# Kernel optimization log

Measured on AMD Instinct MI355X. Metric: run time of the kernel, lower is better.

The kernel has to match this reference:

```python
import jax, jax.numpy as jnp
import numpy as np

D_MODEL = 16
D_STATE = 8
D_CONV = 2
EXPAND = 1
HEADDIM = 2
CHUNK = 64
D_INNER = EXPAND * D_MODEL          # 16
NHEADS = D_INNER // HEADDIM         # 8
CONV_DIM = D_INNER + 2 * D_STATE    # 32
D_IN_PROJ = 2 * D_INNER + 2 * D_STATE + NHEADS  # 56
OBS_DIM = 32
N_ACTIONS = 16
T_LEN = 4096
BATCH = 32


def setup_inputs() -> dict:
    key = jax.random.key(0)
    ks = jax.random.split(key, 16)
    return {
        "obs": jax.random.normal(ks[0], (T_LEN, BATCH, OBS_DIM), jnp.float32),
        "W_in": jax.random.normal(ks[1], (D_MODEL, OBS_DIM), jnp.float32) * 0.1,
        "b_in": jax.random.normal(ks[2], (D_MODEL,), jnp.float32) * 0.1,
        "in_proj": jax.random.normal(ks[3], (D_IN_PROJ, D_MODEL), jnp.float32) * 0.1,
        "conv_w": jax.random.normal(ks[4], (CONV_DIM, D_CONV), jnp.float32) * 0.2,
        "conv_b": jax.random.normal(ks[5], (CONV_DIM,), jnp.float32) * 0.1,
        "dt_bias": jax.random.normal(ks[6], (NHEADS,), jnp.float32) * 0.1,
        "A_log": jax.random.normal(ks[7], (NHEADS,), jnp.float32) * 0.5,
        "D_skip": jax.random.normal(ks[8], (NHEADS,), jnp.float32) * 0.1,
        "norm_w": jnp.ones((D_INNER,), jnp.float32),
        "out_proj": jax.random.normal(ks[9], (D_MODEL, D_INNER), jnp.float32) * 0.1,
        "W_out": jax.random.normal(ks[10], (N_ACTIONS, D_MODEL), jnp.float32) * 0.1,
        "b_out": jax.random.normal(ks[11], (N_ACTIONS,), jnp.float32) * 0.1,
    }


def _segsum(x):
    # x: (..., T) -> (..., T, T) with out[..., i, j] = sum_{k=j+1..i} x_k (i>=j), else -inf
    T = x.shape[-1]
    xx = jnp.broadcast_to(x[..., None], x.shape + (T,))
    xx = jnp.where(jnp.tril(jnp.ones((T, T), bool), -1), xx, 0.0)
    s = jnp.cumsum(xx, axis=-2)
    return jnp.where(jnp.tril(jnp.ones((T, T), bool), 0), s, -jnp.inf)


def _ssd(x, A, B, C):
    # x: (b, l, h, p); A: (b, l, h); B, C: (b, l, n). Chunked SSD scan.
    b, l, h, p = x.shape
    c = l // CHUNK
    x = x.reshape(b, c, CHUNK, h, p)
    A = A.reshape(b, c, CHUNK, h).transpose(0, 3, 1, 2)       # b h c l
    B = B.reshape(b, c, CHUNK, -1)                            # b c l n
    C = C.reshape(b, c, CHUNK, -1)                            # b c l n
    A_cs = jnp.cumsum(A, axis=-1)                             # b h c l
    L = jnp.exp(_segsum(A))                                   # b h c l l
    Y_diag = jnp.einsum('bcln,bcsn,bhcls,bcshp->bclhp', C, B, L, x)
    decay_states = jnp.exp(A_cs[..., -1:] - A_cs)             # b h c l
    states = jnp.einsum('bcln,bhcl,bclhp->bchpn', B, decay_states, x)
    states = jnp.concatenate([jnp.zeros_like(states[:, :1]), states], axis=1)  # b (c+1) h p n
    decay_chunk = jnp.exp(_segsum(jnp.pad(A_cs[..., -1], ((0, 0), (0, 0), (1, 0)))))  # b h c+1 c+1
    new_states = jnp.einsum('bhzc,bchpn->bzhpn', decay_chunk, states)
    states = new_states[:, :-1]                               # b c h p n
    Y_off = jnp.einsum('bcln,bchpn,bhcl->bclhp', C, states, jnp.exp(A_cs))
    return (Y_diag + Y_off).reshape(b, l, h, p)


def reference(obs, W_in, b_in, in_proj, conv_w, conv_b, dt_bias, A_log, D_skip,
              norm_w, out_proj, W_out, b_out):
    t, Bsz, _ = obs.shape
    # input Linear + ReLU -> (t, B, d_model); rearrange to (B, t, d_model)
    x = jax.nn.relu(obs @ W_in.T + b_in)
    u = x.transpose(1, 0, 2)                                  # (B, t, d_model)
    zxbcdt = u @ in_proj.T                                    # (B, t, 56)
    z = zxbcdt[..., :D_INNER]
    xBC = zxbcdt[..., D_INNER:D_INNER + CONV_DIM]
    dt = jax.nn.softplus(zxbcdt[..., D_INNER + CONV_DIM:] + dt_bias)  # (B, t, h)
    # causal depthwise conv1d (kernel size D_CONV) + SiLU
    xp = jnp.pad(xBC, ((0, 0), (D_CONV - 1, 0), (0, 0)))
    conv = conv_b
    for k in range(D_CONV):
        conv = conv + xp[:, k:k + t] * conv_w[:, k]
    xBC = jax.nn.silu(conv)
    xs = xBC[..., :D_INNER]
    Bm = xBC[..., D_INNER:D_INNER + D_STATE]
    Cm = xBC[..., D_INNER + D_STATE:]
    A = -jnp.exp(A_log)                                       # (h,)
    xh = xs.reshape(Bsz, t, NHEADS, HEADDIM)
    y = _ssd(xh * dt[..., None], A * dt, Bm, Cm)
    y = y + xh * D_skip[None, None, :, None]
    y = y.reshape(Bsz, t, D_INNER)
    # gated RMSNorm
    y = y * jax.nn.silu(z)
    y = y * jax.lax.rsqrt(jnp.mean(y * y, axis=-1, keepdims=True) + 1e-5) * norm_w
    yo = y @ out_proj.T                                       # (B, t, d_model)
    hid = yo.transpose(1, 0, 2).reshape(t * Bsz, D_MODEL)     # (t*B, n_units)
    logits = jax.nn.relu(hid) @ W_out.T + b_out
    return logits.reshape(t, Bsz, -1)
```

## Files before the change

### kernel.cpp

```cpp
#include <hip/hip_runtime.h>

#define T_LEN  4096
#define BATCHN 32
#define NROWS  (T_LEN*BATCHN)
#define CHUNKL 64
#define NCHUNK (T_LEN/CHUNKL)

#define SIN_STRIDE 52
#define SY_STRIDE  28

typedef float4 f4;

__device__ __forceinline__ float fsilu(float x){ return x / (1.f + __expf(-x)); }
__device__ __forceinline__ float fsoftplus(float x){ return (x > 20.f) ? x : log1pf(__expf(x)); }

__device__ __forceinline__ float group8_sum(float v){
  v += __shfl_xor(v, 1);
  v += __shfl_xor(v, 2);
  v += __shfl_xor(v, 4);
  return v;
}

__global__ __launch_bounds__(256) void k1_proj(
    const float* __restrict__ obs, const float* __restrict__ W_in,
    const float* __restrict__ b_in, const float* __restrict__ in_proj,
    const float* __restrict__ dt_bias,
    float* __restrict__ z_g, float* __restrict__ xbc_g, float* __restrict__ dt_g)
{
  int r = blockIdx.x*256 + threadIdx.x;
  float o[32];
  const f4* op = (const f4*)(obs + (size_t)r*32);
  #pragma unroll
  for (int j=0;j<8;j++){ f4 v = op[j]; o[4*j]=v.x; o[4*j+1]=v.y; o[4*j+2]=v.z; o[4*j+3]=v.w; }
  float x[16];
  #pragma unroll
  for (int i=0;i<16;i++){
    float a = b_in[i];
    #pragma unroll
    for (int k=0;k<32;k++) a += o[k]*W_in[i*32+k];
    x[i] = a > 0.f ? a : 0.f;
  }
  float acc[56];
  #pragma unroll
  for (int j=0;j<56;j++){
    float a = 0.f;
    #pragma unroll
    for (int k=0;k<16;k++) a += x[k]*in_proj[j*16+k];
    acc[j] = a;
  }
  f4* zo = (f4*)(z_g + (size_t)r*16);
  #pragma unroll
  for (int j=0;j<4;j++) zo[j] = make_float4(acc[4*j],acc[4*j+1],acc[4*j+2],acc[4*j+3]);
  f4* xo = (f4*)(xbc_g + (size_t)r*32);
  #pragma unroll
  for (int j=0;j<8;j++) xo[j] = make_float4(acc[16+4*j],acc[17+4*j],acc[18+4*j],acc[19+4*j]);
  float dtv[8];
  #pragma unroll
  for (int k=0;k<8;k++) dtv[k] = fsoftplus(acc[48+k] + dt_bias[k]);
  f4* dto = (f4*)(dt_g + (size_t)r*8);
  dto[0] = make_float4(dtv[0],dtv[1],dtv[2],dtv[3]);
  dto[1] = make_float4(dtv[4],dtv[5],dtv[6],dtv[7]);
}

__global__ __launch_bounds__(64) void k2_scan(
    const float* __restrict__ xbc_g, const float* __restrict__ dt_g,
    const float* __restrict__ conv_w, const float* __restrict__ conv_b,
    const float* __restrict__ A_log, const float* __restrict__ D_skip,
    float* __restrict__ yl_g, float* __restrict__ ea_g, float* __restrict__ cm_g,
    float* __restrict__ sloc_g, float* __restrict__ p_g)
{
  __shared__ float s_in[CHUNKL*SIN_STRIDE];
  __shared__ float s_y[CHUNKL*SY_STRIDE];
  int bid = blockIdx.x;
  int b = bid & 31, c = bid >> 5;
  int l = threadIdx.x;
  int t = c*CHUNKL + l;
  size_t r = (size_t)t*BATCHN + b;

  float xb[32], pv[32], dtv[8];
  {
    const f4* xp = (const f4*)(xbc_g + r*32);
    #pragma unroll
    for (int j=0;j<8;j++){ f4 v=xp[j]; xb[4*j]=v.x; xb[4*j+1]=v.y; xb[4*j+2]=v.z; xb[4*j+3]=v.w; }
    if (t == 0) {
      #pragma unroll
      for (int j=0;j<32;j++) pv[j]=0.f;
    } else {
      const f4* pp = (const f4*)(xbc_g + (r-BATCHN)*32);
      #pragma unroll
      for (int j=0;j<8;j++){ f4 v=pp[j]; pv[4*j]=v.x; pv[4*j+1]=v.y; pv[4*j+2]=v.z; pv[4*j+3]=v.w; }
    }
    const f4* dp = (const f4*)(dt_g + r*8);
    f4 d0=dp[0], d1=dp[1];
    dtv[0]=d0.x; dtv[1]=d0.y; dtv[2]=d0.z; dtv[3]=d0.w;
    dtv[4]=d1.x; dtv[5]=d1.y; dtv[6]=d1.z; dtv[7]=d1.w;
  }
  float sv[32];
  #pragma unroll
  for (int ch=0; ch<32; ch++){
    float cv = conv_b[ch] + pv[ch]*conv_w[ch*2] + xb[ch]*conv_w[ch*2+1];
    sv[ch] = fsilu(cv);
  }
  float xskip[16], cmv[8];
  #pragma unroll
  for (int i=0;i<16;i++) xskip[i] = sv[i]*D_skip[i>>1];
  #pragma unroll
  for (int n=0;n<8;n++) cmv[n] = sv[24+n];
  {
    float row[48];
    #pragma unroll
    for (int n=0;n<8;n++){ row[2*n]=sv[16+n]; row[2*n+1]=sv[24+n]; }
    #pragma unroll
    for (int h=0;h<8;h++){
      float dth = dtv[h];
      row[16+4*h]   = sv[2*h]*dth;
      row[16+4*h+1] = sv[2*h+1]*dth;
      row[16+4*h+2] = __expf(-__expf(A_log[h])*dth);
      row[16+4*h+3] = 0.f;
    }
    f4* sr = (f4*)&s_in[l*SIN_STRIDE];
    #pragma unroll
    for (int j=0;j<12;j++) sr[j] = make_float4(row[4*j],row[4*j+1],row[4*j+2],row[4*j+3]);
  }
  __syncthreads();

  int h = l >> 3, n = l & 7;
  float s0=0.f, s1=0.f, ep=1.f;
  #pragma unroll 8
  for (int tt=0; tt<CHUNKL; tt++){
    float2 bcv = *(const float2*)&s_in[tt*SIN_STRIDE + 2*n];
    f4 xd = *(const f4*)&s_in[tt*SIN_STRIDE + 16 + 4*h];
    s0 = xd.z*s0 + xd.x*bcv.x;
    s1 = xd.z*s1 + xd.y*bcv.x;
    float y0 = group8_sum(s0*bcv.y);
    float y1 = group8_sum(s1*bcv.y);
    ep *= xd.z;
    if (n == 0){
      *(float2*)&s_y[tt*SY_STRIDE + 2*h] = make_float2(y0, y1);
      s_y[tt*SY_STRIDE + 16 + h] = ep;
    }
  }
  {
    size_t sb = ((size_t)(c*32+b)*8 + h)*16 + n;
    sloc_g[sb]   = s0;
    sloc_g[sb+8] = s1;
    if (n == 0) p_g[(size_t)(c*32+b)*8 + h] = ep;
  }
  __syncthreads();

  {
    f4* yo = (f4*)(yl_g + r*16);
    #pragma unroll
    for (int j=0;j<4;j++){
      f4 v = *(const f4*)&s_y[l*SY_STRIDE + 4*j];
      v.x += xskip[4*j]; v.y += xskip[4*j+1]; v.z += xskip[4*j+2]; v.w += xskip[4*j+3];
      yo[j] = v;
    }
    f4* eo = (f4*)(ea_g + r*8);
    eo[0] = *(const f4*)&s_y[l*SY_STRIDE + 16];
    eo[1] = *(const f4*)&s_y[l*SY_STRIDE + 20];
    f4* co = (f4*)(cm_g + r*8);
    co[0] = make_float4(cmv[0],cmv[1],cmv[2],cmv[3]);
    co[1] = make_float4(cmv[4],cmv[5],cmv[6],cmv[7]);
  }
}

__global__ __launch_bounds__(256) void k3_chunkscan(
    const float* __restrict__ sloc_g, const float* __restrict__ p_g,
    float* __restrict__ sinit_g)
{
  int idx = blockIdx.x*256 + threadIdx.x;
  int bh = idx >> 4, pn = idx & 15;
  float s = 0.f;
  #pragma unroll 8
  for (int c=0; c<NCHUNK; c++){
    size_t o = (size_t)c*256 + bh;
    float slc = sloc_g[o*16 + pn];
    float pc  = p_g[o];
    sinit_g[o*16 + pn] = s;
    s = pc*s + slc;
  }
}

__global__ __launch_bounds__(256) void k4_final(
    const float* __restrict__ yl_g, const float* __restrict__ ea_g,
    const float* __restrict__ cm_g, const float* __restrict__ z_g,
    const float* __restrict__ sinit_g,
    const float* __restrict__ norm_w, const float* __restrict__ out_proj,
    const float* __restrict__ W_out, const float* __restrict__ b_out,
    float* __restrict__ out)
{
  int r = blockIdx.x*256 + threadIdx.x;
  int t = r >> 5, b = r & 31, c = t >> 6;
  float y[16], cm[8], ea[8];
  {
    const f4* yp = (const f4*)(yl_g + (size_t)r*16);
    #pragma unroll
    for (int j=0;j<4;j++){ f4 v=yp[j]; y[4*j]=v.x; y[4*j+1]=v.y; y[4*j+2]=v.z; y[4*j+3]=v.w; }
    const f4* cp = (const f4*)(cm_g + (size_t)r*8);
    f4 c0=cp[0], c1=cp[1];
    cm[0]=c0.x; cm[1]=c0.y; cm[2]=c0.z; cm[3]=c0.w; cm[4]=c1.x; cm[5]=c1.y; cm[6]=c1.z; cm[7]=c1.w;
    const f4* epp = (const f4*)(ea_g + (size_t)r*8);
    f4 e0=epp[0], e1=epp[1];
    ea[0]=e0.x; ea[1]=e0.y; ea[2]=e0.z; ea[3]=e0.w; ea[4]=e1.x; ea[5]=e1.y; ea[6]=e1.z; ea[7]=e1.w;
  }
  {
    const float* sb = sinit_g + (size_t)c*4096 + (size_t)b*128;
    #pragma unroll
    for (int h=0; h<8; h++){
      f4 a0 = *(const f4*)(sb + h*16);
      f4 a1 = *(const f4*)(sb + h*16 + 4);
      f4 b0 = *(const f4*)(sb + h*16 + 8);
      f4 b1 = *(const f4*)(sb + h*16 + 12);
      float d0 = cm[0]*a0.x + cm[1]*a0.y + cm[2]*a0.z + cm[3]*a0.w
               + cm[4]*a1.x + cm[5]*a1.y + cm[6]*a1.z + cm[7]*a1.w;
      float d1 = cm[0]*b0.x + cm[1]*b0.y + cm[2]*b0.z + cm[3]*b0.w
               + cm[4]*b1.x + cm[5]*b1.y + cm[6]*b1.z + cm[7]*b1.w;
      y[2*h]   += ea[h]*d0;
      y[2*h+1] += ea[h]*d1;
    }
  }
  float g[16];
  {
    const f4* zp = (const f4*)(z_g + (size_t)r*16);
    #pragma unroll
    for (int j=0;j<4;j++){
      f4 v = zp[j];
      g[4*j]   = y[4*j]  *fsilu(v.x);
      g[4*j+1] = y[4*j+1]*fsilu(v.y);
      g[4*j+2] = y[4*j+2]*fsilu(v.z);
      g[4*j+3] = y[4*j+3]*fsilu(v.w);
    }
  }
  float ss = 0.f;
  #pragma unroll
  for (int i=0;i<16;i++) ss += g[i]*g[i];
  float rinv = rsqrtf(ss*(1.f/16.f) + 1e-5f);
  float gn[16];
  #pragma unroll
  for (int i=0;i<16;i++) gn[i] = g[i]*rinv*norm_w[i];
  float ro[16];
  #pragma unroll
  for (int j=0;j<16;j++){
    float a = 0.f;
    #pragma unroll
    for (int i=0;i<16;i++) a += gn[i]*out_proj[j*16+i];
    ro[j] = a > 0.f ? a : 0.f;
  }
  f4* oo = (f4*)(out + (size_t)r*16);
  #pragma unroll
  for (int q=0;q<4;q++){
    float lo[4];
    #pragma unroll
    for (int kk=0;kk<4;kk++){
      int k = q*4+kk;
      float a = b_out[k];
      #pragma unroll
      for (int j=0;j<16;j++) a += ro[j]*W_out[k*16+j];
      lo[kk] = a;
    }
    oo[q] = make_float4(lo[0],lo[1],lo[2],lo[3]);
  }
}

extern "C" void kernel_launch(void* const* d_in, const int* in_sizes, int n_in,
                              void* d_out, int out_size, void* d_ws, size_t ws_size,
                              hipStream_t stream)
{
  const float* obs     = (const float*)d_in[0];
  const float* W_in    = (const float*)d_in[1];
  const float* b_in    = (const float*)d_in[2];
  const float* in_proj = (const float*)d_in[3];
  const float* conv_w  = (const float*)d_in[4];
  const float* conv_b  = (const float*)d_in[5];
  const float* dt_bias = (const float*)d_in[6];
  const float* A_log   = (const float*)d_in[7];
  const float* D_skip  = (const float*)d_in[8];
  const float* norm_w  = (const float*)d_in[9];
  const float* out_prj = (const float*)d_in[10];
  const float* W_out   = (const float*)d_in[11];
  const float* b_out   = (const float*)d_in[12];
  float* out = (float*)d_out;

  float* ws     = (float*)d_ws;
  float* z_g    = ws;
  float* xbc_g  = z_g    + (size_t)NROWS*16;
  float* dt_g   = xbc_g  + (size_t)NROWS*32;
  float* yl_g   = dt_g   + (size_t)NROWS*8;
  float* ea_g   = yl_g   + (size_t)NROWS*16;
  float* cm_g   = ea_g   + (size_t)NROWS*8;
  float* sloc_g = cm_g   + (size_t)NROWS*8;
  float* p_g    = sloc_g + (size_t)NCHUNK*256*16;
  float* sinit_g= p_g    + (size_t)NCHUNK*256;

  k1_proj<<<NROWS/256, 256, 0, stream>>>(obs, W_in, b_in, in_proj, dt_bias, z_g, xbc_g, dt_g);
  k2_scan<<<BATCHN*NCHUNK, 64, 0, stream>>>(xbc_g, dt_g, conv_w, conv_b, A_log, D_skip,
                                            yl_g, ea_g, cm_g, sloc_g, p_g);
  k3_chunkscan<<<16, 256, 0, stream>>>(sloc_g, p_g, sinit_g);
  k4_final<<<NROWS/256, 256, 0, stream>>>(yl_g, ea_g, cm_g, z_g, sinit_g,
                                          norm_w, out_prj, W_out, b_out, out);
}
```

Measured before the change: 155.2 us.

## Fuse input projection into chunk scan kernel, recompute conv halo row

The projection kernel is merged into the scan kernel. Each thread now computes its own row's input projection, passes the xBC values to its neighbour through shared memory for the causal conv, and writes only z to global. The halo row before each chunk is recomputed by a few threads, which adds three extra barriers. This drops the global round trip of xbc and dt plus one launch, at the cost of running the projection inside 64-thread blocks with higher register pressure.

```diff
diff --git a/kernel.cpp b/kernel.cpp
--- a/kernel.cpp
+++ b/kernel.cpp
@@ -21,52 +21,14 @@
   return v;
 }
 
-__global__ __launch_bounds__(256) void k1_proj(
+__global__ __launch_bounds__(64) void f12_scan(
     const float* __restrict__ obs, const float* __restrict__ W_in,
     const float* __restrict__ b_in, const float* __restrict__ in_proj,
     const float* __restrict__ dt_bias,
-    float* __restrict__ z_g, float* __restrict__ xbc_g, float* __restrict__ dt_g)
-{
-  int r = blockIdx.x*256 + threadIdx.x;
-  float o[32];
-  const f4* op = (const f4*)(obs + (size_t)r*32);
-  #pragma unroll
-  for (int j=0;j<8;j++){ f4 v = op[j]; o[4*j]=v.x; o[4*j+1]=v.y; o[4*j+2]=v.z; o[4*j+3]=v.w; }
-  float x[16];
-  #pragma unroll
-  for (int i=0;i<16;i++){
-    float a = b_in[i];
-    #pragma unroll
-    for (int k=0;k<32;k++) a += o[k]*W_in[i*32+k];
-    x[i] = a > 0.f ? a : 0.f;
-  }
-  float acc[56];
-  #pragma unroll
-  for (int j=0;j<56;j++){
-    float a = 0.f;
-    #pragma unroll
-    for (int k=0;k<16;k++) a += x[k]*in_proj[j*16+k];
-    acc[j] = a;
-  }
-  f4* zo = (f4*)(z_g + (size_t)r*16);
-  #pragma unroll
-  for (int j=0;j<4;j++) zo[j] = make_float4(acc[4*j],acc[4*j+1],acc[4*j+2],acc[4*j+3]);
-  f4* xo = (f4*)(xbc_g + (size_t)r*32);
-  #pragma unroll
-  for (int j=0;j<8;j++) xo[j] = make_float4(acc[16+4*j],acc[17+4*j],acc[18+4*j],acc[19+4*j]);
-  float dtv[8];
-  #pragma unroll
-  for (int k=0;k<8;k++) dtv[k] = fsoftplus(acc[48+k] + dt_bias[k]);
-  f4* dto = (f4*)(dt_g + (size_t)r*8);
-  dto[0] = make_float4(dtv[0],dtv[1],dtv[2],dtv[3]);
-  dto[1] = make_float4(dtv[4],dtv[5],dtv[6],dtv[7]);
-}
-
-__global__ __launch_bounds__(64) void k2_scan(
-    const float* __restrict__ xbc_g, const float* __restrict__ dt_g,
     const float* __restrict__ conv_w, const float* __restrict__ conv_b,
     const float* __restrict__ A_log, const float* __restrict__ D_skip,
-    float* __restrict__ yl_g, float* __restrict__ ea_g, float* __restrict__ cm_g,
+    float* __restrict__ z_g, float* __restrict__ yl_g,
+    float* __restrict__ ea_g, float* __restrict__ cm_g,
     float* __restrict__ sloc_g, float* __restrict__ p_g)
 {
   __shared__ float s_in[CHUNKL*SIN_STRIDE];
@@ -77,28 +39,80 @@
   int t = c*CHUNKL + l;
   size_t r = (size_t)t*BATCHN + b;
 
-  float xb[32], pv[32], dtv[8];
-  {
-    const f4* xp = (const f4*)(xbc_g + r*32);
-    #pragma unroll
-    for (int j=0;j<8;j++){ f4 v=xp[j]; xb[4*j]=v.x; xb[4*j+1]=v.y; xb[4*j+2]=v.z; xb[4*j+3]=v.w; }
-    if (t == 0) {
-      #pragma unroll
-      for (int j=0;j<32;j++) pv[j]=0.f;
-    } else {
-      const f4* pp = (const f4*)(xbc_g + (r-BATCHN)*32);
-      #pragma unroll
-      for (int j=0;j<8;j++){ f4 v=pp[j]; pv[4*j]=v.x; pv[4*j+1]=v.y; pv[4*j+2]=v.z; pv[4*j+3]=v.w; }
-    }
-    const f4* dp = (const f4*)(dt_g + r*8);
-    f4 d0=dp[0], d1=dp[1];
-    dtv[0]=d0.x; dtv[1]=d0.y; dtv[2]=d0.z; dtv[3]=d0.w;
-    dtv[4]=d1.x; dtv[5]=d1.y; dtv[6]=d1.z; dtv[7]=d1.w;
-  }
+  float o[32];
+  {
+    const f4* op = (const f4*)(obs + r*32);
+    #pragma unroll
+    for (int j=0;j<8;j++){ f4 v = op[j]; o[4*j]=v.x; o[4*j+1]=v.y; o[4*j+2]=v.z; o[4*j+3]=v.w; }
+  }
+  float x[16];
+  #pragma unroll
+  for (int i=0;i<16;i++){
+    float a = b_in[i];
+    #pragma unroll
+    for (int k=0;k<32;k++) a += o[k]*W_in[i*32+k];
+    x[i] = a > 0.f ? a : 0.f;
+  }
+  float acc[56];
+  #pragma unroll
+  for (int j=0;j<56;j++){
+    float a = 0.f;
+    #pragma unroll
+    for (int k=0;k<16;k++) a += x[k]*in_proj[j*16+k];
+    acc[j] = a;
+  }
+  {
+    f4* zo = (f4*)(z_g + (size_t)r*16);
+    #pragma unroll
+    for (int j=0;j<4;j++) zo[j] = make_float4(acc[4*j],acc[4*j+1],acc[4*j+2],acc[4*j+3]);
+  }
+  float dtv[8];
+  #pragma unroll
+  for (int k=0;k<8;k++) dtv[k] = fsoftplus(acc[48+k] + dt_bias[k]);
+
+  {
+    f4* sr = (f4*)&s_in[l*SIN_STRIDE];
+    #pragma unroll
+    for (int j=0;j<8;j++) sr[j] = make_float4(acc[16+4*j],acc[17+4*j],acc[18+4*j],acc[19+4*j]);
+  }
+  if (c > 0 && l < 32){
+    size_t rh = ((size_t)(c*CHUNKL) - 1)*BATCHN + b;
+    s_y[l] = obs[rh*32 + l];
+  }
+  __syncthreads();
+
+  if (c > 0 && l < 16){
+    float a = b_in[l];
+    #pragma unroll
+    for (int k=0;k<32;k++) a += s_y[k]*W_in[l*32+k];
+    s_y[32+l] = a > 0.f ? a : 0.f;
+  }
+  __syncthreads();
+  if (c > 0 && l < 32){
+    float a = 0.f;
+    #pragma unroll
+    for (int k=0;k<16;k++) a += s_y[32+k]*in_proj[(16+l)*16+k];
+    s_y[48+l] = a;
+  }
+  __syncthreads();
+
+  float pv[32];
+  if (t == 0){
+    #pragma unroll
+    for (int j=0;j<32;j++) pv[j]=0.f;
+  } else if (l == 0){
+    #pragma unroll
+    for (int j=0;j<8;j++){ f4 v = *(const f4*)&s_y[48+4*j]; pv[4*j]=v.x; pv[4*j+1]=v.y; pv[4*j+2]=v.z; pv[4*j+3]=v.w; }
+  } else {
+    #pragma unroll
+    for (int j=0;j<8;j++){ f4 v = *(const f4*)&s_in[(l-1)*SIN_STRIDE + 4*j]; pv[4*j]=v.x; pv[4*j+1]=v.y; pv[4*j+2]=v.z; pv[4*j+3]=v.w; }
+  }
+  __syncthreads();
+
   float sv[32];
   #pragma unroll
   for (int ch=0; ch<32; ch++){
-    float cv = conv_b[ch] + pv[ch]*conv_w[ch*2] + xb[ch]*conv_w[ch*2+1];
+    float cv = conv_b[ch] + pv[ch]*conv_w[ch*2] + acc[16+ch]*conv_w[ch*2+1];
     sv[ch] = fsilu(cv);
   }
   float xskip[16], cmv[8];
@@ -284,18 +298,16 @@
 
   float* ws     = (float*)d_ws;
   float* z_g    = ws;
-  float* xbc_g  = z_g    + (size_t)NROWS*16;
-  float* dt_g   = xbc_g  + (size_t)NROWS*32;
-  float* yl_g   = dt_g   + (size_t)NROWS*8;
+  float* yl_g   = z_g    + (size_t)NROWS*16;
   float* ea_g   = yl_g   + (size_t)NROWS*16;
   float* cm_g   = ea_g   + (size_t)NROWS*8;
   float* sloc_g = cm_g   + (size_t)NROWS*8;
   float* p_g    = sloc_g + (size_t)NCHUNK*256*16;
   float* sinit_g= p_g    + (size_t)NCHUNK*256;
 
-  k1_proj<<<NROWS/256, 256, 0, stream>>>(obs, W_in, b_in, in_proj, dt_bias, z_g, xbc_g, dt_g);
-  k2_scan<<<BATCHN*NCHUNK, 64, 0, stream>>>(xbc_g, dt_g, conv_w, conv_b, A_log, D_skip,
-                                            yl_g, ea_g, cm_g, sloc_g, p_g);
+  f12_scan<<<BATCHN*NCHUNK, 64, 0, stream>>>(obs, W_in, b_in, in_proj, dt_bias,
+                                             conv_w, conv_b, A_log, D_skip,
+                                             z_g, yl_g, ea_g, cm_g, sloc_g, p_g);
   k3_chunkscan<<<16, 256, 0, stream>>>(sloc_g, p_g, sinit_g);
   k4_final<<<NROWS/256, 256, 0, stream>>>(yl_g, ea_g, cm_g, z_g, sinit_g,
                                           norm_w, out_prj, W_out, b_out, out);
```

Result: faster. 151.4 us (-2.4%).
